# Kernel tuning notes

Hardware: AMD Instinct MI355X
Metric: run time of the kernel (lower is better)

## Reference

```python
import jax, jax.numpy as jnp
import numpy as np

H = 16          # num_heads
EPS = 1e-5      # LayerNorm eps (torch default)


def _layernorm(x, g, b):
    m = jnp.mean(x, axis=-1, keepdims=True)
    v = jnp.mean((x - m) ** 2, axis=-1, keepdims=True)
    return (x - m) * jax.lax.rsqrt(v + EPS) * g + b


def setup_inputs() -> dict:
    key = jax.random.key(0)
    ks = jax.random.split(key, 16)
    B, S, D, F = 4, 1024, 1024, 4096
    s = 0.02
    inp = {
        "x": jax.random.normal(ks[0], (B, S, D), jnp.float32),
        "attn_bias": jax.random.normal(ks[1], (B - 1, H), jnp.float32),
        "mask": jax.random.randint(ks[2], (B, 1, S, S), 0, 2).astype(jnp.float32),
        "ln1_g": jnp.ones((D,), jnp.float32),
        "ln1_b": jnp.zeros((D,), jnp.float32),
        "Wq": jax.random.normal(ks[3], (D, D), jnp.float32) * s,
        "bq": jnp.zeros((D,), jnp.float32),
        "Wk": jax.random.normal(ks[4], (D, D), jnp.float32) * s,
        "bk": jnp.zeros((D,), jnp.float32),
        "Wv": jax.random.normal(ks[5], (D, D), jnp.float32) * s,
        "bv": jnp.zeros((D,), jnp.float32),
        "Wo": jax.random.normal(ks[6], (D, D), jnp.float32) * s,
        "bo": jnp.zeros((D,), jnp.float32),
        "ln2_g": jnp.ones((D,), jnp.float32),
        "ln2_b": jnp.zeros((D,), jnp.float32),
        "W1": jax.random.normal(ks[7], (D, F), jnp.float32) * s,
        "b1": jnp.zeros((F,), jnp.float32),
        "W2": jax.random.normal(ks[8], (F, D), jnp.float32) * s,
        "b2": jnp.zeros((D,), jnp.float32),
    }
    return inp


def reference(x, attn_bias, mask, ln1_g, ln1_b, Wq, bq, Wk, bk, Wv, bv, Wo, bo,
              ln2_g, ln2_b, W1, b1, W2, b2):
    B, S, D = x.shape
    d = D // H
    scale = d ** -0.5

    # ---- self-attention block ----
    y = _layernorm(x, ln1_g, ln1_b)
    q = (y @ Wq + bq).reshape(B, S, H, d).transpose(0, 2, 1, 3) * scale  # [B,H,S,d]
    k = (y @ Wk + bk).reshape(B, S, H, d).transpose(0, 2, 1, 3)
    v = (y @ Wv + bv).reshape(B, S, H, d).transpose(0, 2, 1, 3)

    scores = jnp.einsum("bhqd,bhkd->bhqk", q, k)                         # [B,H,S,S]
    # per-batch additive bias applied to batches 1: only (as in torch x[1:] += bias)
    scores = scores.at[1:].add(attn_bias[:, :, None, None])
    # multiplicative mask + large-negative additive mask where mask <= 0
    scores = scores * mask + jnp.where(mask > 0.0, 0.0, -1e9)
    attn = jax.nn.softmax(scores, axis=-1)

    ctx = jnp.einsum("bhqk,bhkd->bhqd", attn, v)                          # [B,H,S,d]
    ctx = ctx.transpose(0, 2, 1, 3).reshape(B, S, D)
    x = x + (ctx @ Wo + bo)

    # ---- FFN block ----
    y = _layernorm(x, ln2_g, ln2_b)
    y = jax.nn.gelu(y @ W1 + b1, approximate=False) @ W2 + b2
    return x + y
```

## Files before the change

### kernel.cpp

```cpp
#include <hip/hip_runtime.h>
#include <hip/hip_bf16.h>
#include <math.h>

typedef __attribute__((ext_vector_type(8))) __bf16 bf16x8;
typedef __attribute__((ext_vector_type(4))) float f32x4;
typedef __hip_bfloat16 bf16;

#define D_MODEL 1024
#define F_FFN   4096
#define NHEAD   16
#define HDIM    64
#define SEQ     1024
#define BATCH   4

static __device__ __forceinline__ unsigned short bf_bits(bf16 h) {
  return __builtin_bit_cast(unsigned short, h);
}

template <int N>
static __device__ __forceinline__ void vwait() {
  asm volatile("s_waitcnt vmcnt(%0)" :: "n"(N) : "memory");
}

__global__ __launch_bounds__(1024) void transpose_cast_kernel(
    const float* __restrict__ W, bf16* __restrict__ Wt, int K, int N) {
  __shared__ float tile[32][33];
  int nb = blockIdx.x * 32, kb = blockIdx.y * 32;
  int tx = threadIdx.x, ty = threadIdx.y;
  tile[ty][tx] = W[(size_t)(kb + ty) * N + nb + tx];
  __syncthreads();
  Wt[(size_t)(nb + ty) * K + kb + tx] = __float2bfloat16(tile[tx][ty]);
}

__global__ __launch_bounds__(256) void maskbits_kernel(
    const float* __restrict__ mask, unsigned* __restrict__ mbits) {
  int gw = (blockIdx.x * 256 + threadIdx.x) >> 6;
  int lane = threadIdx.x & 63;
  const float4 m = reinterpret_cast<const float4*>(mask)[(size_t)gw * 64 + lane];
  unsigned long long b0 = __ballot(m.x > 0.f);
  unsigned long long b1 = __ballot(m.y > 0.f);
  unsigned long long b2 = __ballot(m.z > 0.f);
  unsigned long long b3 = __ballot(m.w > 0.f);
  if (lane < 8) {
    unsigned v = 0;
#pragma unroll
    for (int i = 0; i < 8; ++i) {
      int srcl = lane * 8 + i;
      v |= (((unsigned)(b0 >> srcl) & 1u) << (i * 4 + 0));
      v |= (((unsigned)(b1 >> srcl) & 1u) << (i * 4 + 1));
      v |= (((unsigned)(b2 >> srcl) & 1u) << (i * 4 + 2));
      v |= (((unsigned)(b3 >> srcl) & 1u) << (i * 4 + 3));
    }
    mbits[(size_t)gw * 8 + lane] = v;
  }
}

__global__ __launch_bounds__(256) void layernorm_kernel(
    const float* __restrict__ x, const float* __restrict__ g,
    const float* __restrict__ bt, bf16* __restrict__ y) {
  int row = blockIdx.x;
  int tid = threadIdx.x;
  const float* xr = x + (size_t)row * D_MODEL;
  float4 v = reinterpret_cast<const float4*>(xr)[tid];
  float s  = v.x + v.y + v.z + v.w;
  float s2 = v.x * v.x + v.y * v.y + v.z * v.z + v.w * v.w;
  for (int o = 32; o; o >>= 1) { s += __shfl_xor(s, o); s2 += __shfl_xor(s2, o); }
  __shared__ float r1[4], r2[4];
  int wid = tid >> 6, lane = tid & 63;
  if (lane == 0) { r1[wid] = s; r2[wid] = s2; }
  __syncthreads();
  float tot  = r1[0] + r1[1] + r1[2] + r1[3];
  float tot2 = r2[0] + r2[1] + r2[2] + r2[3];
  float mean = tot * (1.f / D_MODEL);
  float var  = tot2 * (1.f / D_MODEL) - mean * mean;
  float rstd = rsqrtf(var + 1e-5f);
  float4 gg = reinterpret_cast<const float4*>(g)[tid];
  float4 bb = reinterpret_cast<const float4*>(bt)[tid];
  ushort4 o;
  o.x = bf_bits(__float2bfloat16((v.x - mean) * rstd * gg.x + bb.x));
  o.y = bf_bits(__float2bfloat16((v.y - mean) * rstd * gg.y + bb.y));
  o.z = bf_bits(__float2bfloat16((v.z - mean) * rstd * gg.z + bb.z));
  o.w = bf_bits(__float2bfloat16((v.w - mean) * rstd * gg.w + bb.w));
  reinterpret_cast<ushort4*>(y + (size_t)row * D_MODEL)[tid] = o;
}

enum { MODE_QKV = 0, MODE_O = 1, MODE_GELU = 2, MODE_OUT = 3 };

template <int MODE, int TN>
__global__ __launch_bounds__(256, 3) void gemm_bt_kernel(
    const bf16* __restrict__ A, const bf16* __restrict__ Bt,
    int M, int N, int K,
    const float* __restrict__ bias0, const float* __restrict__ bias1,
    const float* __restrict__ bias2,
    const float* __restrict__ resid,
    bf16* __restrict__ out_q, bf16* __restrict__ out_k, bf16* __restrict__ out_vt,
    bf16* __restrict__ out_bf, float* __restrict__ out_f) {
  constexpr int TM = 128, TK = 32, R = 3;
  constexpr int NI = TN / 32;
  constexpr int LA = 2, LB = TN / 64;
  constexpr int L  = LA + LB;
  __shared__ bf16 As[R][TM * TK];
  __shared__ bf16 Bs[R][TN * TK];
  int tid = threadIdx.x;
  int wid = tid >> 6, lane = tid & 63;
  int nwg = gridDim.x * gridDim.y;
  int lin = blockIdx.y * gridDim.x + blockIdx.x;
  int swz = (lin & 7) * (nwg >> 3) + (lin >> 3);
  int bxi = swz % gridDim.x, byi = swz / gridDim.x;
  int bm = byi * TM, bn = bxi * TN;
  int wm = (wid >> 1) * 64, wn = (wid & 1) * (TN / 2);
  int lrow = lane & 15, lg = lane >> 4;
  int r16 = lane >> 2;
  int sg  = (lane & 3) ^ ((lane >> 3) & 3);
  const bf16* Asrc = A  + (size_t)bm * K + sg * 8;
  const bf16* Bsrc = Bt + (size_t)bn * K + sg * 8;
  f32x4 acc[4][NI] = {};
  const int NT = K / TK;

  auto stage = [&](int t, int slot) {
    int k0 = t * TK;
#pragma unroll
    for (int j = 0; j < LA; ++j) {
      int chunk = wid * LA + j;
      __builtin_amdgcn_global_load_lds(
          (const __attribute__((address_space(1))) void*)(
              Asrc + (size_t)(chunk * 16 + r16) * K + k0),
          (__attribute__((address_space(3))) void*)(&As[slot][chunk * 512]), 16, 0, 0);
    }
#pragma unroll
    for (int j = 0; j < LB; ++j) {
      int chunk = wid * LB + j;
      __builtin_amdgcn_global_load_lds(
          (const __attribute__((address_space(1))) void*)(
              Bsrc + (size_t)(chunk * 16 + r16) * K + k0),
          (__attribute__((address_space(3))) void*)(&Bs[slot][chunk * 512]), 16, 0, 0);
    }
  };

  int sw = (lg ^ ((lrow >> 1) & 3)) << 4;
  stage(0, 0);
  stage(1, 1);
  int rslot = 0, wslot = 2;
  for (int t = 0; t < NT; ++t) {
    if (t < NT - 1) vwait<L>();
    else            vwait<0>();
    __builtin_amdgcn_s_barrier();
    const char* as = (const char*)As[rslot];
    const char* bs = (const char*)Bs[rslot];
    bf16x8 af[4], bfr[NI];
#pragma unroll
    for (int mi = 0; mi < 4; ++mi)
      af[mi] = *reinterpret_cast<const bf16x8*>(as + (wm + mi * 16 + lrow) * 64 + sw);
#pragma unroll
    for (int ni = 0; ni < NI; ++ni)
      bfr[ni] = *reinterpret_cast<const bf16x8*>(bs + (wn + ni * 16 + lrow) * 64 + sw);
    if (t + 2 < NT) stage(t + 2, wslot);
#pragma unroll
    for (int mi = 0; mi < 4; ++mi)
#pragma unroll
      for (int ni = 0; ni < NI; ++ni)
        acc[mi][ni] = __builtin_amdgcn_mfma_f32_16x16x32_bf16(af[mi], bfr[ni], acc[mi][ni], 0, 0, 0);
    rslot = (rslot == R - 1) ? 0 : rslot + 1;
    wslot = (wslot == R - 1) ? 0 : wslot + 1;
  }

#pragma unroll
  for (int mi = 0; mi < 4; ++mi) {
#pragma unroll
    for (int ni = 0; ni < NI; ++ni) {
#pragma unroll
      for (int r = 0; r < 4; ++r) {
        int row = bm + wm + mi * 16 + lg * 4 + r;
        int col = bn + wn + ni * 16 + lrow;
        float v = acc[mi][ni][r];
        if (MODE == MODE_QKV) {
          if (col < 1024) {
            out_q[(size_t)row * 1024 + col] = __float2bfloat16((v + bias0[col]) * 0.125f);
          } else if (col < 2048) {
            out_k[(size_t)row * 1024 + (col - 1024)] = __float2bfloat16(v + bias1[col - 1024]);
          } else {
            int d = col - 2048;
            int b = row >> 10;
            int s = row & 1023;
            out_vt[((size_t)(b << 10) + d) * 1024 + s] = __float2bfloat16(v + bias2[d]);
          }
        } else if (MODE == MODE_O) {
          out_f[(size_t)row * N + col] = resid[(size_t)row * N + col] + v + bias0[col];
        } else if (MODE == MODE_GELU) {
          float t = v + bias0[col];
          out_bf[(size_t)row * N + col] =
              __float2bfloat16(0.5f * t * (1.f + erff(t * 0.70710678118654752f)));
        } else {
          out_f[(size_t)row * N + col] = resid[(size_t)row * N + col] + v + bias0[col];
        }
      }
    }
  }
}

#define KVB 64
__global__ __launch_bounds__(256) void attn_kernel(
    const bf16* __restrict__ q, const bf16* __restrict__ k,
    const bf16* __restrict__ vt, const unsigned* __restrict__ mbits,
    bf16* __restrict__ ctx) {
  __shared__ bf16 Kt[2][KVB * 64];
  __shared__ bf16 Vt[2][KVB * 64];
  __shared__ bf16 P[4][16 * 64];
  int tid = threadIdx.x, wid = tid >> 6, lane = tid & 63;
  int blk = (blockIdx.x & 7) * 128 + (blockIdx.x >> 3);
  int qblk = blk & 15, h = (blk >> 4) & 15, b = blk >> 8;
  int qs = qblk * 64 + wid * 16;
  int lrow = lane & 15, lg = lane >> 4;

  size_t qoff = ((size_t)(b * SEQ + qs + lrow)) * D_MODEL + h * HDIM;
  bf16x8 qa0 = *reinterpret_cast<const bf16x8*>(q + qoff + lg * 8);
  bf16x8 qa1 = *reinterpret_cast<const bf16x8*>(q + qoff + 32 + lg * 8);

  float ps[4] = {0.f, 0.f, 0.f, 0.f};
  f32x4 O[4] = {};
  const unsigned* mb = mbits + ((size_t)(b * SEQ + qs + lg * 4)) * 32;
  bf16* Pw = P[wid];

  int rr = lane >> 3;
  int sg8 = (lane & 7) ^ rr;
  const bf16* kb_src = k + ((size_t)b * SEQ) * D_MODEL + h * HDIM + sg8 * 8;
  const bf16* vb_src = vt + ((size_t)(b * D_MODEL + h * HDIM)) * SEQ + sg8 * 8;

#define STAGE(KT2, BUF)                                                              \
  {                                                                                  \
    int ks2 = (KT2) * KVB;                                                           \
    _Pragma("unroll") for (int j = 0; j < 2; ++j) {                                  \
      int chunk = wid * 2 + j;                                                       \
      __builtin_amdgcn_global_load_lds(                                              \
          (const __attribute__((address_space(1))) void*)(                           \
              kb_src + (size_t)(ks2 + chunk * 8 + rr) * D_MODEL),                    \
          (__attribute__((address_space(3))) void*)(&Kt[BUF][chunk * 512]), 16, 0, 0);\
      __builtin_amdgcn_global_load_lds(                                              \
          (const __attribute__((address_space(1))) void*)(                           \
              vb_src + (size_t)(chunk * 8 + rr) * SEQ + ks2),                        \
          (__attribute__((address_space(3))) void*)(&Vt[BUF][chunk * 512]), 16, 0, 0);\
    }                                                                                \
  }

  STAGE(0, 0);
  for (int kt = 0; kt < SEQ / KVB; ++kt) {
    int cur = kt & 1;
    __syncthreads();
    if (kt < SEQ / KVB - 1) STAGE(kt + 1, cur ^ 1);

    f32x4 sc[4];
#pragma unroll
    for (int c = 0; c < 4; ++c) {
      int krow = c * 16 + lrow;
      const char* kp = (const char*)&Kt[cur][krow * 64];
      bf16x8 kb0 = *reinterpret_cast<const bf16x8*>(kp + ((lg ^ (krow & 7)) << 4));
      bf16x8 kb1 = *reinterpret_cast<const bf16x8*>(kp + ((((lg + 4) & 7) ^ (krow & 7)) << 4));
      f32x4 z = {0.f, 0.f, 0.f, 0.f};
      sc[c] = __builtin_amdgcn_mfma_f32_16x16x32_bf16(qa0, kb0, z, 0, 0, 0);
      sc[c] = __builtin_amdgcn_mfma_f32_16x16x32_bf16(qa1, kb1, sc[c], 0, 0, 0);
    }

#pragma unroll
    for (int r = 0; r < 4; ++r) {
      uint2 w = *reinterpret_cast<const uint2*>(mb + (size_t)r * 32 + kt * 2);
      int prow = lg * 4 + r;
      char* pb = (char*)Pw + prow * 128;
#pragma unroll
      for (int c = 0; c < 4; ++c) {
        unsigned wsel = (c >= 2) ? w.y : w.x;
        unsigned keep = (wsel >> ((c & 1) * 16 + lrow)) & 1u;
        float p = keep ? __expf(sc[c][r]) : 0.f;
        ps[r] += p;
        int pcol = c * 16 + lrow;
        *(__bf16*)(pb + (((pcol >> 3) ^ (prow & 7)) << 4) + (pcol & 7) * 2) =
            __float2bfloat16(p);
      }
    }

    const char* pbase = (const char*)Pw + lrow * 128;
    bf16x8 pa0 = *reinterpret_cast<const bf16x8*>(pbase + ((lg ^ (lrow & 7)) << 4));
    bf16x8 pa1 = *reinterpret_cast<const bf16x8*>(pbase + ((((lg + 4) & 7) ^ (lrow & 7)) << 4));
#pragma unroll
    for (int nb = 0; nb < 4; ++nb) {
      int vrow = nb * 16 + lrow;
      const char* vp = (const char*)&Vt[cur][vrow * 64];
      bf16x8 vb0 = *reinterpret_cast<const bf16x8*>(vp + ((lg ^ (vrow & 7)) << 4));
      bf16x8 vb1 = *reinterpret_cast<const bf16x8*>(vp + ((((lg + 4) & 7) ^ (vrow & 7)) << 4));
      O[nb] = __builtin_amdgcn_mfma_f32_16x16x32_bf16(pa0, vb0, O[nb], 0, 0, 0);
      O[nb] = __builtin_amdgcn_mfma_f32_16x16x32_bf16(pa1, vb1, O[nb], 0, 0, 0);
    }
  }
#undef STAGE

#pragma unroll
  for (int o = 1; o < 16; o <<= 1)
#pragma unroll
    for (int r = 0; r < 4; ++r) ps[r] += __shfl_xor(ps[r], o);
#pragma unroll
  for (int nb = 0; nb < 4; ++nb)
#pragma unroll
    for (int r = 0; r < 4; ++r) {
      int qg = qs + lg * 4 + r;
      ctx[((size_t)(b * SEQ + qg)) * D_MODEL + h * HDIM + nb * 16 + lrow] =
          __float2bfloat16(O[nb][r] / ps[r]);
    }
}

extern "C" void kernel_launch(void* const* d_in, const int* in_sizes, int n_in,
                              void* d_out, int out_size, void* d_ws, size_t ws_size,
                              hipStream_t stream) {
  const float* x        = (const float*)d_in[0];
  const float* mask     = (const float*)d_in[2];
  const float* ln1_g    = (const float*)d_in[3];
  const float* ln1_b    = (const float*)d_in[4];
  const float* Wq       = (const float*)d_in[5];
  const float* bq       = (const float*)d_in[6];
  const float* Wk       = (const float*)d_in[7];
  const float* bk       = (const float*)d_in[8];
  const float* Wv       = (const float*)d_in[9];
  const float* bv       = (const float*)d_in[10];
  const float* Wo       = (const float*)d_in[11];
  const float* bo       = (const float*)d_in[12];
  const float* ln2_g    = (const float*)d_in[13];
  const float* ln2_b    = (const float*)d_in[14];
  const float* W1       = (const float*)d_in[15];
  const float* b1       = (const float*)d_in[16];
  const float* W2       = (const float*)d_in[17];
  const float* b2       = (const float*)d_in[18];
  float* out            = (float*)d_out;

  char* w = (char*)d_ws;
  const size_t MB = 1u << 20;
  bf16*     y      = (bf16*)(w + 0);
  bf16*     qb     = (bf16*)(w + 8 * MB);
  bf16*     kb     = (bf16*)(w + 16 * MB);
  bf16*     vt     = (bf16*)(w + 24 * MB);
  bf16*     hbuf   = (bf16*)(w + 0);
  bf16*     Wqkv_t = (bf16*)(w + 32 * MB);
  bf16*     Wo_t   = (bf16*)(w + 38 * MB);
  bf16*     W1_t   = (bf16*)(w + 40 * MB);
  bf16*     W2_t   = (bf16*)(w + 48 * MB);
  bf16*     ctx    = (bf16*)(w + 56 * MB);
  float*    x2     = (float*)(w + 64 * MB);
  unsigned* mbits  = (unsigned*)(w + 64 * MB);
  bf16*     y2     = (bf16*)(w + 80 * MB);
  (void)in_sizes; (void)n_in; (void)out_size; (void)ws_size;

  dim3 tb(32, 32);
  transpose_cast_kernel<<<dim3(32, 32), tb, 0, stream>>>(Wq, Wqkv_t, 1024, 1024);
  transpose_cast_kernel<<<dim3(32, 32), tb, 0, stream>>>(Wk, Wqkv_t + 1024 * 1024, 1024, 1024);
  transpose_cast_kernel<<<dim3(32, 32), tb, 0, stream>>>(Wv, Wqkv_t + 2 * 1024 * 1024, 1024, 1024);
  transpose_cast_kernel<<<dim3(32, 32), tb, 0, stream>>>(Wo, Wo_t, 1024, 1024);
  transpose_cast_kernel<<<dim3(128, 32), tb, 0, stream>>>(W1, W1_t, 1024, 4096);
  transpose_cast_kernel<<<dim3(32, 128), tb, 0, stream>>>(W2, W2_t, 4096, 1024);

  maskbits_kernel<<<4096, 256, 0, stream>>>(mask, mbits);

  layernorm_kernel<<<4096, 256, 0, stream>>>(x, ln1_g, ln1_b, y);

  gemm_bt_kernel<MODE_QKV, 128><<<dim3(24, 32), 256, 0, stream>>>(
      y, Wqkv_t, 4096, 3072, 1024, bq, bk, bv, nullptr, qb, kb, vt, nullptr, nullptr);

  attn_kernel<<<1024, 256, 0, stream>>>(qb, kb, vt, mbits, ctx);

  gemm_bt_kernel<MODE_O, 64><<<dim3(16, 32), 256, 0, stream>>>(
      ctx, Wo_t, 4096, 1024, 1024, bo, nullptr, nullptr, x,
      nullptr, nullptr, nullptr, nullptr, x2);

  layernorm_kernel<<<4096, 256, 0, stream>>>(x2, ln2_g, ln2_b, y2);

  gemm_bt_kernel<MODE_GELU, 128><<<dim3(32, 32), 256, 0, stream>>>(
      y2, W1_t, 4096, 4096, 1024, b1, nullptr, nullptr, nullptr,
      nullptr, nullptr, nullptr, hbuf, nullptr);

  gemm_bt_kernel<MODE_OUT, 64><<<dim3(16, 32), 256, 0, stream>>>(
      hbuf, W2_t, 4096, 1024, 4096, b2, nullptr, nullptr, x2,
      nullptr, nullptr, nullptr, nullptr, out);
}
```

Measured before the change: 261.7 us.

## Enlarge GEMM tiles to 256 rows, widen attention blocks, fuse prep kernels

Merges the six weight transpose-cast launches and the mask bit-packing launch into a single prep kernel. The GEMM becomes a 512-thread, 256-row-tile kernel with one load per thread per stage and s_setprio around the MFMA loop. The attention kernel moves to 512 threads covering 128 query rows per block, halving the grid. The aim is fewer launches and more reuse of each B tile per block, at the cost of fewer workgroups (down to 256 for the N=1024 GEMMs) and higher per-block LDS use.

```diff
diff --git a/kernel.cpp b/kernel.cpp
--- a/kernel.cpp
+++ b/kernel.cpp
@@ -22,36 +22,63 @@
   asm volatile("s_waitcnt vmcnt(%0)" :: "n"(N) : "memory");
 }
 
-__global__ __launch_bounds__(1024) void transpose_cast_kernel(
-    const float* __restrict__ W, bf16* __restrict__ Wt, int K, int N) {
+static __device__ __forceinline__ void gload_lds16(const bf16* src, bf16* dst) {
+  __builtin_amdgcn_global_load_lds(
+      (const __attribute__((address_space(1))) void*)src,
+      (__attribute__((address_space(3))) void*)dst, 16, 0, 0);
+}
+
+__global__ __launch_bounds__(1024) void prep_kernel(
+    const float* __restrict__ Wq, const float* __restrict__ Wk,
+    const float* __restrict__ Wv, const float* __restrict__ Wo,
+    const float* __restrict__ W1, const float* __restrict__ W2,
+    const float* __restrict__ mask,
+    bf16* __restrict__ Wqkv_t, bf16* __restrict__ Wo_t,
+    bf16* __restrict__ W1_t, bf16* __restrict__ W2_t,
+    unsigned* __restrict__ mbits) {
   __shared__ float tile[32][33];
-  int nb = blockIdx.x * 32, kb = blockIdx.y * 32;
-  int tx = threadIdx.x, ty = threadIdx.y;
-  tile[ty][tx] = W[(size_t)(kb + ty) * N + nb + tx];
-  __syncthreads();
-  Wt[(size_t)(nb + ty) * K + kb + tx] = __float2bfloat16(tile[tx][ty]);
-}
-
-__global__ __launch_bounds__(256) void maskbits_kernel(
-    const float* __restrict__ mask, unsigned* __restrict__ mbits) {
-  int gw = (blockIdx.x * 256 + threadIdx.x) >> 6;
-  int lane = threadIdx.x & 63;
-  const float4 m = reinterpret_cast<const float4*>(mask)[(size_t)gw * 64 + lane];
-  unsigned long long b0 = __ballot(m.x > 0.f);
-  unsigned long long b1 = __ballot(m.y > 0.f);
-  unsigned long long b2 = __ballot(m.z > 0.f);
-  unsigned long long b3 = __ballot(m.w > 0.f);
-  if (lane < 8) {
-    unsigned v = 0;
-#pragma unroll
-    for (int i = 0; i < 8; ++i) {
-      int srcl = lane * 8 + i;
-      v |= (((unsigned)(b0 >> srcl) & 1u) << (i * 4 + 0));
-      v |= (((unsigned)(b1 >> srcl) & 1u) << (i * 4 + 1));
-      v |= (((unsigned)(b2 >> srcl) & 1u) << (i * 4 + 2));
-      v |= (((unsigned)(b3 >> srcl) & 1u) << (i * 4 + 3));
-    }
-    mbits[(size_t)gw * 8 + lane] = v;
+  int bid = blockIdx.x;
+  int tid = threadIdx.x;
+  if (bid < 12288) {
+    const float* W; bf16* Wt; int K, N, tx32, ty32;
+    if (bid < 4096) {
+      int w = bid >> 10;
+      W  = (w == 0) ? Wq : (w == 1) ? Wk : (w == 2) ? Wv : Wo;
+      Wt = (w < 3) ? Wqkv_t + (size_t)w * 1024 * 1024 : Wo_t;
+      K = 1024; N = 1024;
+      int t = bid & 1023; tx32 = t & 31; ty32 = t >> 5;
+    } else if (bid < 8192) {
+      W = W1; Wt = W1_t; K = 1024; N = 4096;
+      int t = bid - 4096; tx32 = t & 127; ty32 = t >> 7;
+    } else {
+      W = W2; Wt = W2_t; K = 4096; N = 1024;
+      int t = bid - 8192; tx32 = t & 31; ty32 = t >> 5;
+    }
+    int nb = tx32 * 32, kb = ty32 * 32;
+    int tx = tid & 31, ty = tid >> 5;
+    tile[ty][tx] = W[(size_t)(kb + ty) * N + nb + tx];
+    __syncthreads();
+    Wt[(size_t)(nb + ty) * K + kb + tx] = __float2bfloat16(tile[tx][ty]);
+  } else {
+    int gw = ((bid - 12288) * 1024 + tid) >> 6;
+    int lane = tid & 63;
+    const float4 m = reinterpret_cast<const float4*>(mask)[(size_t)gw * 64 + lane];
+    unsigned long long b0 = __ballot(m.x > 0.f);
+    unsigned long long b1 = __ballot(m.y > 0.f);
+    unsigned long long b2 = __ballot(m.z > 0.f);
+    unsigned long long b3 = __ballot(m.w > 0.f);
+    if (lane < 8) {
+      unsigned v = 0;
+#pragma unroll
+      for (int i = 0; i < 8; ++i) {
+        int srcl = lane * 8 + i;
+        v |= (((unsigned)(b0 >> srcl) & 1u) << (i * 4 + 0));
+        v |= (((unsigned)(b1 >> srcl) & 1u) << (i * 4 + 1));
+        v |= (((unsigned)(b2 >> srcl) & 1u) << (i * 4 + 2));
+        v |= (((unsigned)(b3 >> srcl) & 1u) << (i * 4 + 3));
+      }
+      mbits[(size_t)gw * 8 + lane] = v;
+    }
   }
 }
 
@@ -87,7 +114,7 @@
 enum { MODE_QKV = 0, MODE_O = 1, MODE_GELU = 2, MODE_OUT = 3 };
 
 template <int MODE, int TN>
-__global__ __launch_bounds__(256, 3) void gemm_bt_kernel(
+__global__ __launch_bounds__(512, 4) void gemm256_kernel(
     const bf16* __restrict__ A, const bf16* __restrict__ Bt,
     int M, int N, int K,
     const float* __restrict__ bias0, const float* __restrict__ bias1,
@@ -95,45 +122,38 @@
     const float* __restrict__ resid,
     bf16* __restrict__ out_q, bf16* __restrict__ out_k, bf16* __restrict__ out_vt,
     bf16* __restrict__ out_bf, float* __restrict__ out_f) {
-  constexpr int TM = 128, TK = 32, R = 3;
-  constexpr int NI = TN / 32;
-  constexpr int LA = 2, LB = TN / 64;
-  constexpr int L  = LA + LB;
-  __shared__ bf16 As[R][TM * TK];
-  __shared__ bf16 Bs[R][TN * TK];
+  constexpr int R = 3;
+  constexpr int NF = TN / 32;
+  __shared__ bf16 AS[R][256 * 32];
+  __shared__ bf16 BS[R][TN * 32];
   int tid = threadIdx.x;
   int wid = tid >> 6, lane = tid & 63;
+  int wm4 = wid >> 1, wn2 = wid & 1;
+  int lrow = lane & 15, lg = lane >> 4;
   int nwg = gridDim.x * gridDim.y;
   int lin = blockIdx.y * gridDim.x + blockIdx.x;
   int swz = (lin & 7) * (nwg >> 3) + (lin >> 3);
   int bxi = swz % gridDim.x, byi = swz / gridDim.x;
-  int bm = byi * TM, bn = bxi * TN;
-  int wm = (wid >> 1) * 64, wn = (wid & 1) * (TN / 2);
-  int lrow = lane & 15, lg = lane >> 4;
-  int r16 = lane >> 2;
-  int sg  = (lane & 3) ^ ((lane >> 3) & 3);
+  int bm = byi * 256, bn = bxi * TN;
+  int srow = tid >> 2;
+  int sg = (tid & 3) ^ ((tid >> 3) & 3);
   const bf16* Asrc = A  + (size_t)bm * K + sg * 8;
   const bf16* Bsrc = Bt + (size_t)bn * K + sg * 8;
-  f32x4 acc[4][NI] = {};
-  const int NT = K / TK;
+  f32x4 acc[4][NF] = {};
+  const int NT = K / 32;
 
   auto stage = [&](int t, int slot) {
-    int k0 = t * TK;
-#pragma unroll
-    for (int j = 0; j < LA; ++j) {
-      int chunk = wid * LA + j;
-      __builtin_amdgcn_global_load_lds(
-          (const __attribute__((address_space(1))) void*)(
-              Asrc + (size_t)(chunk * 16 + r16) * K + k0),
-          (__attribute__((address_space(3))) void*)(&As[slot][chunk * 512]), 16, 0, 0);
-    }
-#pragma unroll
-    for (int j = 0; j < LB; ++j) {
-      int chunk = wid * LB + j;
-      __builtin_amdgcn_global_load_lds(
-          (const __attribute__((address_space(1))) void*)(
-              Bsrc + (size_t)(chunk * 16 + r16) * K + k0),
-          (__attribute__((address_space(3))) void*)(&Bs[slot][chunk * 512]), 16, 0, 0);
+    int k0 = t * 32;
+#pragma unroll
+    for (int j = 0; j < 2; ++j) {
+      int row = j * 128 + srow;
+      gload_lds16(Asrc + (size_t)row * K + k0, &AS[slot][(j * 512 + tid) * 8]);
+    }
+    if (TN == 128) {
+      gload_lds16(Bsrc + (size_t)srow * K + k0, &BS[slot][tid * 8]);
+    } else {
+      if (wid < 4)
+        gload_lds16(Bsrc + (size_t)srow * K + k0, &BS[slot][tid * 8]);
     }
   };
 
@@ -142,37 +162,43 @@
   stage(1, 1);
   int rslot = 0, wslot = 2;
   for (int t = 0; t < NT; ++t) {
-    if (t < NT - 1) vwait<L>();
-    else            vwait<0>();
+    if (t < NT - 1) {
+      if (TN == 128) { vwait<3>(); }
+      else { if (wid < 4) vwait<3>(); else vwait<2>(); }
+    } else {
+      vwait<0>();
+    }
     __builtin_amdgcn_s_barrier();
-    const char* as = (const char*)As[rslot];
-    const char* bs = (const char*)Bs[rslot];
-    bf16x8 af[4], bfr[NI];
-#pragma unroll
-    for (int mi = 0; mi < 4; ++mi)
-      af[mi] = *reinterpret_cast<const bf16x8*>(as + (wm + mi * 16 + lrow) * 64 + sw);
-#pragma unroll
-    for (int ni = 0; ni < NI; ++ni)
-      bfr[ni] = *reinterpret_cast<const bf16x8*>(bs + (wn + ni * 16 + lrow) * 64 + sw);
+    const char* as = (const char*)AS[rslot];
+    const char* bs = (const char*)BS[rslot];
+    bf16x8 af[4], bfr[NF];
+#pragma unroll
+    for (int f = 0; f < 4; ++f)
+      af[f] = *reinterpret_cast<const bf16x8*>(as + (wm4 * 64 + f * 16 + lrow) * 64 + sw);
+#pragma unroll
+    for (int g = 0; g < NF; ++g)
+      bfr[g] = *reinterpret_cast<const bf16x8*>(bs + (wn2 * (TN / 2) + g * 16 + lrow) * 64 + sw);
     if (t + 2 < NT) stage(t + 2, wslot);
-#pragma unroll
-    for (int mi = 0; mi < 4; ++mi)
-#pragma unroll
-      for (int ni = 0; ni < NI; ++ni)
-        acc[mi][ni] = __builtin_amdgcn_mfma_f32_16x16x32_bf16(af[mi], bfr[ni], acc[mi][ni], 0, 0, 0);
+    __builtin_amdgcn_s_setprio(1);
+#pragma unroll
+    for (int f = 0; f < 4; ++f)
+#pragma unroll
+      for (int g = 0; g < NF; ++g)
+        acc[f][g] = __builtin_amdgcn_mfma_f32_16x16x32_bf16(af[f], bfr[g], acc[f][g], 0, 0, 0);
+    __builtin_amdgcn_s_setprio(0);
     rslot = (rslot == R - 1) ? 0 : rslot + 1;
     wslot = (wslot == R - 1) ? 0 : wslot + 1;
   }
 
 #pragma unroll
-  for (int mi = 0; mi < 4; ++mi) {
-#pragma unroll
-    for (int ni = 0; ni < NI; ++ni) {
+  for (int f = 0; f < 4; ++f) {
+#pragma unroll
+    for (int g = 0; g < NF; ++g) {
 #pragma unroll
       for (int r = 0; r < 4; ++r) {
-        int row = bm + wm + mi * 16 + lg * 4 + r;
-        int col = bn + wn + ni * 16 + lrow;
-        float v = acc[mi][ni][r];
+        int row = bm + wm4 * 64 + f * 16 + lg * 4 + r;
+        int col = bn + wn2 * (TN / 2) + g * 16 + lrow;
+        float v = acc[f][g][r];
         if (MODE == MODE_QKV) {
           if (col < 1024) {
             out_q[(size_t)row * 1024 + col] = __float2bfloat16((v + bias0[col]) * 0.125f);
@@ -184,12 +210,10 @@
             int s = row & 1023;
             out_vt[((size_t)(b << 10) + d) * 1024 + s] = __float2bfloat16(v + bias2[d]);
           }
-        } else if (MODE == MODE_O) {
-          out_f[(size_t)row * N + col] = resid[(size_t)row * N + col] + v + bias0[col];
         } else if (MODE == MODE_GELU) {
-          float t = v + bias0[col];
+          float tv = v + bias0[col];
           out_bf[(size_t)row * N + col] =
-              __float2bfloat16(0.5f * t * (1.f + erff(t * 0.70710678118654752f)));
+              __float2bfloat16(0.5f * tv * (1.f + erff(tv * 0.70710678118654752f)));
         } else {
           out_f[(size_t)row * N + col] = resid[(size_t)row * N + col] + v + bias0[col];
         }
@@ -199,17 +223,17 @@
 }
 
 #define KVB 64
-__global__ __launch_bounds__(256) void attn_kernel(
+__global__ __launch_bounds__(512) void attn_kernel(
     const bf16* __restrict__ q, const bf16* __restrict__ k,
     const bf16* __restrict__ vt, const unsigned* __restrict__ mbits,
     bf16* __restrict__ ctx) {
   __shared__ bf16 Kt[2][KVB * 64];
   __shared__ bf16 Vt[2][KVB * 64];
-  __shared__ bf16 P[4][16 * 64];
+  __shared__ bf16 P[8][16 * 64];
   int tid = threadIdx.x, wid = tid >> 6, lane = tid & 63;
-  int blk = (blockIdx.x & 7) * 128 + (blockIdx.x >> 3);
-  int qblk = blk & 15, h = (blk >> 4) & 15, b = blk >> 8;
-  int qs = qblk * 64 + wid * 16;
+  int blk = (blockIdx.x & 7) * 64 + (blockIdx.x >> 3);
+  int qblk = blk & 7, h = (blk >> 3) & 15, b = blk >> 7;
+  int qs = qblk * 128 + wid * 16;
   int lrow = lane & 15, lg = lane >> 4;
 
   size_t qoff = ((size_t)(b * SEQ + qs + lrow)) * D_MODEL + h * HDIM;
@@ -226,20 +250,13 @@
   const bf16* kb_src = k + ((size_t)b * SEQ) * D_MODEL + h * HDIM + sg8 * 8;
   const bf16* vb_src = vt + ((size_t)(b * D_MODEL + h * HDIM)) * SEQ + sg8 * 8;
 
-#define STAGE(KT2, BUF)                                                              \
-  {                                                                                  \
-    int ks2 = (KT2) * KVB;                                                           \
-    _Pragma("unroll") for (int j = 0; j < 2; ++j) {                                  \
-      int chunk = wid * 2 + j;                                                       \
-      __builtin_amdgcn_global_load_lds(                                              \
-          (const __attribute__((address_space(1))) void*)(                           \
-              kb_src + (size_t)(ks2 + chunk * 8 + rr) * D_MODEL),                    \
-          (__attribute__((address_space(3))) void*)(&Kt[BUF][chunk * 512]), 16, 0, 0);\
-      __builtin_amdgcn_global_load_lds(                                              \
-          (const __attribute__((address_space(1))) void*)(                           \
-              vb_src + (size_t)(chunk * 8 + rr) * SEQ + ks2),                        \
-          (__attribute__((address_space(3))) void*)(&Vt[BUF][chunk * 512]), 16, 0, 0);\
-    }                                                                                \
+#define STAGE(KT2, BUF)                                                          \
+  {                                                                              \
+    int ks2 = (KT2) * KVB;                                                       \
+    gload_lds16(kb_src + (size_t)(ks2 + wid * 8 + rr) * D_MODEL,                 \
+                &Kt[BUF][wid * 512]);                                            \
+    gload_lds16(vb_src + (size_t)(wid * 8 + rr) * SEQ + ks2,                     \
+                &Vt[BUF][wid * 512]);                                            \
   }
 
   STAGE(0, 0);
@@ -346,34 +363,28 @@
   bf16*     y2     = (bf16*)(w + 80 * MB);
   (void)in_sizes; (void)n_in; (void)out_size; (void)ws_size;
 
-  dim3 tb(32, 32);
-  transpose_cast_kernel<<<dim3(32, 32), tb, 0, stream>>>(Wq, Wqkv_t, 1024, 1024);
-  transpose_cast_kernel<<<dim3(32, 32), tb, 0, stream>>>(Wk, Wqkv_t + 1024 * 1024, 1024, 1024);
-  transpose_cast_kernel<<<dim3(32, 32), tb, 0, stream>>>(Wv, Wqkv_t + 2 * 1024 * 1024, 1024, 1024);
-  transpose_cast_kernel<<<dim3(32, 32), tb, 0, stream>>>(Wo, Wo_t, 1024, 1024);
-  transpose_cast_kernel<<<dim3(128, 32), tb, 0, stream>>>(W1, W1_t, 1024, 4096);
-  transpose_cast_kernel<<<dim3(32, 128), tb, 0, stream>>>(W2, W2_t, 4096, 1024);
-
-  maskbits_kernel<<<4096, 256, 0, stream>>>(mask, mbits);
+  prep_kernel<<<13312, 1024, 0, stream>>>(Wq, Wk, Wv, Wo, W1, W2, mask,
+                                          Wqkv_t, Wo_t, W1_t, W2_t, mbits);
 
   layernorm_kernel<<<4096, 256, 0, stream>>>(x, ln1_g, ln1_b, y);
 
-  gemm_bt_kernel<MODE_QKV, 128><<<dim3(24, 32), 256, 0, stream>>>(
-      y, Wqkv_t, 4096, 3072, 1024, bq, bk, bv, nullptr, qb, kb, vt, nullptr, nullptr);
-
-  attn_kernel<<<1024, 256, 0, stream>>>(qb, kb, vt, mbits, ctx);
-
-  gemm_bt_kernel<MODE_O, 64><<<dim3(16, 32), 256, 0, stream>>>(
+  gemm256_kernel<MODE_QKV, 128><<<dim3(24, 16), 512, 0, stream>>>(
+      y, Wqkv_t, 4096, 3072, 1024, bq, bk, bv, nullptr,
+      qb, kb, vt, nullptr, nullptr);
+
+  attn_kernel<<<512, 512, 0, stream>>>(qb, kb, vt, mbits, ctx);
+
+  gemm256_kernel<MODE_O, 64><<<dim3(16, 16), 512, 0, stream>>>(
       ctx, Wo_t, 4096, 1024, 1024, bo, nullptr, nullptr, x,
       nullptr, nullptr, nullptr, nullptr, x2);
 
   layernorm_kernel<<<4096, 256, 0, stream>>>(x2, ln2_g, ln2_b, y2);
 
-  gemm_bt_kernel<MODE_GELU, 128><<<dim3(32, 32), 256, 0, stream>>>(
+  gemm256_kernel<MODE_GELU, 128><<<dim3(32, 16), 512, 0, stream>>>(
       y2, W1_t, 4096, 4096, 1024, b1, nullptr, nullptr, nullptr,
       nullptr, nullptr, nullptr, hbuf, nullptr);
 
-  gemm_bt_kernel<MODE_OUT, 64><<<dim3(16, 32), 256, 0, stream>>>(
+  gemm256_kernel<MODE_OUT, 64><<<dim3(16, 16), 512, 0, stream>>>(
       hbuf, W2_t, 4096, 1024, 4096, b2, nullptr, nullptr, x2,
       nullptr, nullptr, nullptr, nullptr, out);
 }
```

New measurement: 251.4 us. 3.9% less time.
